# Optimization experiments

Measured on AMD Instinct MI355X. Metric: run time of the kernel, lower is better.

Reference implementation:

```python
import jax, jax.numpy as jnp
import numpy as np

B, P = 16, 1024
D_TIME, NUM_MODS = 8, 22
DIM_S = NUM_MODS + D_TIME + 1  # 31
PHI_W, N_HEADS, DP = 32, 4, 32
PSI_W, PSI_L, RHO_W = 64, 64, 64
SQRT_DP = float(np.sqrt(DP))


def setup_inputs() -> dict:
    key = jax.random.key(0)
    ks = jax.random.split(key, 16)
    rn = lambda k, shape: jax.random.normal(k, shape, jnp.float32) * 0.05
    return dict(
        times=jax.random.uniform(ks[0], (B, P), jnp.float32) * 48.0,
        values=jax.random.normal(ks[1], (B, P), jnp.float32),
        measurements=jax.random.randint(ks[2], (B, P), 0, NUM_MODS + 1),
        non_pad_mask=jnp.ones((B, P, 1), jnp.float32),
        W_psi1=rn(ks[3], (DIM_S, PSI_W)), b_psi1=jnp.zeros((PSI_W,), jnp.float32),
        W_psi2=rn(ks[4], (PSI_W, PSI_L)), b_psi2=jnp.zeros((PSI_L,), jnp.float32),
        W_key=rn(ks[5], (DIM_S + PSI_L, N_HEADS * DP)), b_key=jnp.zeros((N_HEADS * DP,), jnp.float32),
        query=rn(ks[6], (N_HEADS, DP)),
        W_phi1=rn(ks[7], (DIM_S, PHI_W)), b_phi1=jnp.zeros((PHI_W,), jnp.float32),
        W_phi2=rn(ks[8], (PHI_W, PHI_W)), b_phi2=jnp.zeros((PHI_W,), jnp.float32),
        W_rho1=rn(ks[9], (N_HEADS * PHI_W, RHO_W)), b_rho1=jnp.zeros((RHO_W,), jnp.float32),
        W_rho2=rn(ks[10], (RHO_W, RHO_W)), b_rho2=jnp.zeros((RHO_W,), jnp.float32),
    )


def _temporal_enc(times):
    i = np.arange(D_TIME)
    pos_vec = jnp.asarray(10000.0 ** (2.0 * (i // 2) / D_TIME), jnp.float32)
    ang = times[:, :, None] / pos_vec  # [B,P,d_time]
    return jnp.where(jnp.asarray(i % 2 == 0), jnp.sin(ang), jnp.cos(ang))


def reference(times, values, measurements, non_pad_mask,
              W_psi1, b_psi1, W_psi2, b_psi2, W_key, b_key, query,
              W_phi1, b_phi1, W_phi2, b_phi2, W_rho1, b_rho1, W_rho2, b_rho2):
    m = non_pad_mask  # [B,P,1]
    te = _temporal_enc(times)
    oh = jax.nn.one_hot(measurements, NUM_MODS + 1, dtype=jnp.float32)[:, :, 1:]
    x = jnp.concatenate([te, values[:, :, None], oh], axis=-1)  # [B,P,dim_s]

    # CumulativeSetAttentionLayer: psi MLP -> cumulative mean -> keys . query
    psi = jax.nn.relu(jax.nn.relu(x @ W_psi1 + b_psi1) @ W_psi2 + b_psi2)  # [B,P,psi_l]
    cum = jnp.cumsum(psi * m, axis=1) / jnp.cumsum(m, axis=1)
    keys = (jnp.concatenate([x, cum], axis=-1) @ W_key + b_key).reshape(B, P, N_HEADS, DP)
    pre = jnp.einsum('bpmd,md->bpm', keys, query) / SQRT_DP  # [B,P,m]

    # phi MLP
    phi = jax.nn.relu(jax.nn.relu(x @ W_phi1 + b_phi1) @ W_phi2 + b_phi2) * m  # [B,P,phi_w]

    # cumulative softmax weighting (online path)
    cmax = jax.lax.cummax(pre, axis=1)  # [B,P,m], running max for stability
    D = jnp.exp(pre[:, None, :, :] - cmax[:, :, None, :])  # [B,P,Q,m]
    causal = jnp.arange(P)[:, None] >= jnp.arange(P)[None, :]  # keep Q <= P
    D = D * causal[None, :, :, None]
    E = D.sum(axis=2)  # [B,P,m]
    agg = jnp.einsum('bpqm,bqd->bpmd', D, phi) / E[:, :, :, None]
    agg = (agg * m[:, :, :, None]).reshape(B, P, N_HEADS * PHI_W)

    # rho MLP (return_sequences)
    out = jax.nn.relu(jax.nn.relu(agg @ W_rho1 + b_rho1) @ W_rho2 + b_rho2) * m
    return out
```

## Files before the change

kernel.cpp:

```cpp
#include <hip/hip_runtime.h>
#include <hip/hip_bf16.h>

#define B_ 16
#define P_ 1024
#define T_ (B_*P_)
#define CH_ 32
#define CL_ (P_/CH_)

constexpr int OFF_A     = 16;
constexpr int OFF_WPSI1 = 400;
constexpr int OFF_BPSI1 = OFF_WPSI1 + 1984;
constexpr int OFF_WPSI2 = OFF_BPSI1 + 64;
constexpr int OFF_BPSI2 = OFF_WPSI2 + 4096;
constexpr int OFF_WPHI1 = OFF_BPSI2 + 64;
constexpr int OFF_BPHI1 = OFF_WPHI1 + 992;
constexpr int OFF_WPHI2 = OFF_BPHI1 + 32;
constexpr int OFF_BPHI2 = OFF_WPHI2 + 1024;
constexpr int OFF_WRHO1 = OFF_BPHI2 + 32;
constexpr int OFF_BRHO1 = OFF_WRHO1 + 8192;
constexpr int OFF_WRHO2 = OFF_BRHO1 + 64;
constexpr int OFF_BRHO2 = OFF_WRHO2 + 4096;
constexpr int OFF_PHI   = OFF_BRHO2 + 64;
constexpr int OFF_Z     = OFF_PHI   + T_*32;
constexpr int OFF_PREX  = OFF_Z     + T_*4;
constexpr int OFF_EXPW  = OFF_PREX  + T_*4;
constexpr int OFF_CE    = OFF_EXPW  + T_*4;
constexpr int OFF_CS    = OFF_CE    + 2048;

static __device__ __forceinline__ bool detect_f32(const void* mask_raw) {
  return ((*(const unsigned*)mask_raw) & 0xFFFFu) == 0u;
}
static __device__ __forceinline__ float ld_any(const void* src, int i, bool isf32) {
  if (isf32) return ((const float*)src)[i];
  return __bfloat162float(((const __hip_bfloat16*)src)[i]);
}

__global__ __launch_bounds__(256) void s01_prep(
    float* __restrict__ ws, const void* mask,
    const void* Wpsi1, const void* bpsi1, const void* Wpsi2, const void* bpsi2,
    const void* Wkey,  const void* bkey,  const void* query,
    const void* Wphi1, const void* bphi1, const void* Wphi2, const void* bphi2) {
  const bool isf32 = detect_f32(mask);
  if (blockIdx.x < 2) {
    const int gid = blockIdx.x * 256 + threadIdx.x;
    if (gid >= 384) return;
    const float inv_s = 0.17677669529663687f;
    const int h = gid & 3;
    const int j = gid >> 2;
    float s = 0.f;
    if (j < 95) {
      for (int d = 0; d < 32; ++d)
        s += ld_any(Wkey, j * 128 + h * 32 + d, isf32) * ld_any(query, h * 32 + d, isf32);
    } else {
      for (int d = 0; d < 32; ++d)
        s += ld_any(bkey, h * 32 + d, isf32) * ld_any(query, h * 32 + d, isf32);
    }
    ws[OFF_A + gid] = s * inv_s;
    return;
  }
  const int g  = (blockIdx.x - 2) * 256 + threadIdx.x;
  const int gs = (gridDim.x - 2) * 256;
  auto st = [&](int off, const void* src, int n) {
    for (int i = g; i < n; i += gs) ws[off + i] = ld_any(src, i, isf32);
  };
  st(OFF_WPSI1, Wpsi1, 1984); st(OFF_BPSI1, bpsi1, 64);
  st(OFF_WPSI2, Wpsi2, 4096); st(OFF_BPSI2, bpsi2, 64);
  st(OFF_WPHI1, Wphi1, 992);  st(OFF_BPHI1, bphi1, 32);
  st(OFF_WPHI2, Wphi2, 1024); st(OFF_BPHI2, bphi2, 32);
}

__global__ __launch_bounds__(256) void k1_token(float* __restrict__ ws,
                                                const int* __restrict__ measp,
                                                const void* __restrict__ times,
                                                const void* __restrict__ values,
                                                const void* __restrict__ mask) {
  __shared__ float sh1[4][64];
  __shared__ float sg1[4][32];
  const bool isf32 = detect_f32(mask);
  const int tid = threadIdx.x;
  const int wv  = __builtin_amdgcn_readfirstlane(tid >> 6);
  const int j   = tid & 63;
  const int t   = blockIdx.x * 4 + wv;

  const float tval = ld_any(times, t, isf32);
  const float vval = ld_any(values, t, isf32);
  const float mval = ld_any(mask, t, isf32);
  const int   meas = measp[t];
  const float sel  = (meas > 0) ? 1.f : 0.f;
  const int   mrow = (meas > 0) ? (8 + meas) : 0;

  float x[9];
  const float posv[4] = {1.f, 10.f, 100.f, 1000.f};
  #pragma unroll
  for (int k = 0; k < 4; ++k) {
    float s, c;
    __sincosf(tval / posv[k], &s, &c);
    x[2*k] = s; x[2*k+1] = c;
  }
  x[8] = vval;

  float h1 = ws[OFF_BPSI1 + j];
  #pragma unroll
  for (int i = 0; i < 9; ++i) h1 = fmaf(x[i], ws[OFF_WPSI1 + i * 64 + j], h1);
  h1 = fmaf(sel, ws[OFF_WPSI1 + mrow * 64 + j], h1);
  sh1[wv][j] = fmaxf(h1, 0.f);

  if (j < 32) {
    float g1 = ws[OFF_BPHI1 + j];
    #pragma unroll
    for (int i = 0; i < 9; ++i) g1 = fmaf(x[i], ws[OFF_WPHI1 + i * 32 + j], g1);
    g1 = fmaf(sel, ws[OFF_WPHI1 + mrow * 32 + j], g1);
    sg1[wv][j] = fmaxf(g1, 0.f);
  }
  __syncthreads();

  float h2 = ws[OFF_BPSI2 + j];
  #pragma unroll 8
  for (int i = 0; i < 64; ++i) h2 = fmaf(sh1[wv][i], ws[OFF_WPSI2 + i * 64 + j], h2);
  const float q = fmaxf(h2, 0.f) * mval;

  const float* a2 = ws + OFF_A + (31 + j) * 4;
  float z0 = q * a2[0], z1 = q * a2[1], z2 = q * a2[2], z3 = q * a2[3];
  #pragma unroll
  for (int off = 32; off; off >>= 1) {
    z0 += __shfl_xor(z0, off, 64);
    z1 += __shfl_xor(z1, off, 64);
    z2 += __shfl_xor(z2, off, 64);
    z3 += __shfl_xor(z3, off, 64);
  }
  if (j == 0) {
    float* zo = ws + OFF_Z + (size_t)t * 4;
    zo[0] = z0; zo[1] = z1; zo[2] = z2; zo[3] = z3;
  }

  if (j < 32) {
    float g2 = ws[OFF_BPHI2 + j];
    #pragma unroll 8
    for (int i = 0; i < 32; ++i) g2 = fmaf(sg1[wv][i], ws[OFF_WPHI2 + i * 32 + j], g2);
    ws[OFF_PHI + (size_t)t * 32 + j] = fmaxf(g2, 0.f) * mval;
  } else if (j < 36) {
    const int h = j - 32;
    float pr = ws[OFF_A + 380 + h];
    #pragma unroll
    for (int i = 0; i < 9; ++i) pr = fmaf(x[i], ws[OFF_A + i * 4 + h], pr);
    pr = fmaf(sel, ws[OFF_A + mrow * 4 + h], pr);
    ws[OFF_PREX + (size_t)t * 4 + h] = pr;
  }
}

__global__ __launch_bounds__(256) void k2_scanz(float* __restrict__ ws,
                                                const void* __restrict__ mask) {
  const int b    = blockIdx.x;
  const int tid  = threadIdx.x;
  const int lane = tid & 63;
  const int wv   = tid >> 6;
  const bool isf32 = detect_f32(mask);
  __shared__ float swt[4][5];
  __shared__ float smx[4][4];

  const float* zB = ws + OFF_Z + (size_t)b * P_ * 4;
  const int p0 = tid * 4;

  float lc[4], l0[4], l1[4], l2[4], l3[4];
  float c = 0.f, z0 = 0.f, z1 = 0.f, z2 = 0.f, z3 = 0.f;
  const float4* z4 = (const float4*)(zB + (size_t)p0 * 4);
  #pragma unroll
  for (int i = 0; i < 4; ++i) {
    const float4 zv = z4[i];
    c  += ld_any(mask, b * P_ + p0 + i, isf32);
    z0 += zv.x; z1 += zv.y; z2 += zv.z; z3 += zv.w;
    lc[i] = c; l0[i] = z0; l1[i] = z1; l2[i] = z2; l3[i] = z3;
  }

  float rc = c, r0 = z0, r1 = z1, r2 = z2, r3 = z3;
  #pragma unroll
  for (int off = 1; off < 64; off <<= 1) {
    const float uc = __shfl_up(rc, off, 64);
    const float u0 = __shfl_up(r0, off, 64);
    const float u1 = __shfl_up(r1, off, 64);
    const float u2 = __shfl_up(r2, off, 64);
    const float u3 = __shfl_up(r3, off, 64);
    if (lane >= off) { rc += uc; r0 += u0; r1 += u1; r2 += u2; r3 += u3; }
  }
  if (lane == 63) {
    swt[wv][0] = rc; swt[wv][1] = r0; swt[wv][2] = r1; swt[wv][3] = r2; swt[wv][4] = r3;
  }
  __syncthreads();
  #pragma unroll
  for (int w2 = 0; w2 < 3; ++w2) {
    if (wv > w2) {
      rc += swt[w2][0]; r0 += swt[w2][1]; r1 += swt[w2][2];
      r2 += swt[w2][3]; r3 += swt[w2][4];
    }
  }
  const float ec = rc - c, e0 = r0 - z0, e1 = r1 - z1, e2 = r2 - z2, e3 = r3 - z3;

  const float* px = ws + OFF_PREX + (size_t)b * P_ * 4;
  const float4* px4 = (const float4*)(px + (size_t)p0 * 4);
  float pre[4][4];
  float mx0 = -1e30f, mx1 = -1e30f, mx2 = -1e30f, mx3 = -1e30f;
  #pragma unroll
  for (int i = 0; i < 4; ++i) {
    const float inv = 1.f / (ec + lc[i]);
    const float4 pv = px4[i];
    pre[i][0] = pv.x + (e0 + l0[i]) * inv;
    pre[i][1] = pv.y + (e1 + l1[i]) * inv;
    pre[i][2] = pv.z + (e2 + l2[i]) * inv;
    pre[i][3] = pv.w + (e3 + l3[i]) * inv;
    mx0 = fmaxf(mx0, pre[i][0]); mx1 = fmaxf(mx1, pre[i][1]);
    mx2 = fmaxf(mx2, pre[i][2]); mx3 = fmaxf(mx3, pre[i][3]);
  }

  #pragma unroll
  for (int off = 32; off; off >>= 1) {
    mx0 = fmaxf(mx0, __shfl_xor(mx0, off, 64));
    mx1 = fmaxf(mx1, __shfl_xor(mx1, off, 64));
    mx2 = fmaxf(mx2, __shfl_xor(mx2, off, 64));
    mx3 = fmaxf(mx3, __shfl_xor(mx3, off, 64));
  }
  if (lane == 0) { smx[wv][0] = mx0; smx[wv][1] = mx1; smx[wv][2] = mx2; smx[wv][3] = mx3; }
  __syncthreads();
  const float M0 = fmaxf(fmaxf(smx[0][0], smx[1][0]), fmaxf(smx[2][0], smx[3][0]));
  const float M1 = fmaxf(fmaxf(smx[0][1], smx[1][1]), fmaxf(smx[2][1], smx[3][1]));
  const float M2 = fmaxf(fmaxf(smx[0][2], smx[1][2]), fmaxf(smx[2][2], smx[3][2]));
  const float M3 = fmaxf(fmaxf(smx[0][3], smx[1][3]), fmaxf(smx[2][3], smx[3][3]));

  float* eB = ws + OFF_EXPW + (size_t)b * P_ * 4;
  float4* e4 = (float4*)(eB + (size_t)p0 * 4);
  #pragma unroll
  for (int i = 0; i < 4; ++i) {
    float4 ev;
    ev.x = __expf(pre[i][0] - M0);
    ev.y = __expf(pre[i][1] - M1);
    ev.z = __expf(pre[i][2] - M2);
    ev.w = __expf(pre[i][3] - M3);
    e4[i] = ev;
  }
}

__global__ __launch_bounds__(128) void k4a_sums(float* __restrict__ ws) {
  const int ch = blockIdx.x, b = blockIdx.y;
  const int h = threadIdx.x >> 5, d = threadIdx.x & 31;
  const float* eB   = ws + OFF_EXPW + (size_t)b * P_ * 4;
  const float* phiB = ws + OFF_PHI  + (size_t)b * P_ * 32;

  float E = 0.f, S = 0.f;
  const int pbeg = ch * CL_;
  #pragma unroll 4
  for (int p = pbeg; p < pbeg + CL_; ++p) {
    const float e  = eB[p * 4 + h];
    const float ph = phiB[p * 32 + d];
    E += e;
    S = fmaf(e, ph, S);
  }
  const int base = (b * CH_ + ch) * 4 + h;
  if (d == 0) ws[OFF_CE + base] = E;
  ws[OFF_CS + base * 32 + d] = S;
}

__global__ __launch_bounds__(256) void k45_fused(float* __restrict__ ws,
    const void* __restrict__ mask,
    const void* __restrict__ Wrho1, const void* __restrict__ brho1,
    const void* __restrict__ Wrho2, const void* __restrict__ brho2,
    void* __restrict__ out) {
  __shared__ float sW1[8192];
  __shared__ float sAgg[32][128];
  __shared__ float sH1[32][64];
  const int ch = blockIdx.x, b = blockIdx.y;
  const int tid = threadIdx.x;
  const bool isf32 = detect_f32(mask);
  const int pbeg = ch * CL_;

  if (tid < 128) {
    const int h = tid >> 5, d = tid & 31;
    const float* eB   = ws + OFF_EXPW + (size_t)b * P_ * 4;
    const float* phiB = ws + OFF_PHI  + (size_t)b * P_ * 32;
    float E = 0.f, S = 0.f;
    for (int c2 = 0; c2 < ch; ++c2) {
      const int base2 = (b * CH_ + c2) * 4 + h;
      E += ws[OFF_CE + base2];
      S += ws[OFF_CS + base2 * 32 + d];
    }
    #pragma unroll 4
    for (int p = pbeg; p < pbeg + CL_; ++p) {
      const float e  = eB[p * 4 + h];
      const float ph = phiB[p * 32 + d];
      E += e;
      S = fmaf(e, ph, S);
      sAgg[p - pbeg][h * 32 + d] = (S / E) * ld_any(mask, b * P_ + p, isf32);
    }
  } else {
    for (int i = tid - 128; i < 8192; i += 128) sW1[i] = ld_any(Wrho1, i, isf32);
  }
  __syncthreads();

  const int j = tid & 63, qw = tid >> 6;
  const float b1 = ld_any(brho1, j, isf32);
  float acc[8];
  #pragma unroll
  for (int k = 0; k < 8; ++k) acc[k] = b1;
  for (int i4 = 0; i4 < 32; ++i4) {
    const float w0 = sW1[(i4 * 4 + 0) * 64 + j];
    const float w1 = sW1[(i4 * 4 + 1) * 64 + j];
    const float w2 = sW1[(i4 * 4 + 2) * 64 + j];
    const float w3 = sW1[(i4 * 4 + 3) * 64 + j];
    #pragma unroll
    for (int k = 0; k < 8; ++k) {
      const float4 a = *(const float4*)&sAgg[qw * 8 + k][i4 * 4];
      acc[k] = fmaf(a.w, w3, fmaf(a.z, w2, fmaf(a.y, w1, fmaf(a.x, w0, acc[k]))));
    }
  }
  #pragma unroll
  for (int k = 0; k < 8; ++k) sH1[qw * 8 + k][j] = fmaxf(acc[k], 0.f);
  __syncthreads();

  const float b2 = ld_any(brho2, j, isf32);
  float o[8];
  #pragma unroll
  for (int k = 0; k < 8; ++k) o[k] = b2;
  if (isf32) {
    const float* W2 = (const float*)Wrho2;
    #pragma unroll 4
    for (int i = 0; i < 64; ++i) {
      const float w = W2[i * 64 + j];
      #pragma unroll
      for (int k = 0; k < 8; ++k) o[k] = fmaf(sH1[qw * 8 + k][i], w, o[k]);
    }
  } else {
    const __hip_bfloat16* W2 = (const __hip_bfloat16*)Wrho2;
    #pragma unroll 4
    for (int i = 0; i < 64; ++i) {
      const float w = __bfloat162float(W2[i * 64 + j]);
      #pragma unroll
      for (int k = 0; k < 8; ++k) o[k] = fmaf(sH1[qw * 8 + k][i], w, o[k]);
    }
  }

  const int t0 = b * P_ + pbeg + qw * 8;
  #pragma unroll
  for (int k = 0; k < 8; ++k) {
    const float mv = ld_any(mask, t0 + k, isf32);
    const float v  = fmaxf(o[k], 0.f) * mv;
    if (isf32) {
      ((float*)out)[(size_t)(t0 + k) * 64 + j] = v;
    } else {
      ((__hip_bfloat16*)out)[(size_t)(t0 + k) * 64 + j] = __float2bfloat16(v);
    }
  }
}

extern "C" void kernel_launch(void* const* d_in, const int* in_sizes, int n_in,
                              void* d_out, int out_size, void* d_ws, size_t ws_size,
                              hipStream_t stream) {
  const int* meas = (const int*)d_in[2];
  const void* times = d_in[0];
  const void* values = d_in[1];
  const void* mask = d_in[3];
  float* ws = (float*)d_ws;

  s01_prep<<<10, 256, 0, stream>>>(ws, mask,
                                   d_in[4], d_in[5], d_in[6], d_in[7],
                                   d_in[8], d_in[9], d_in[10],
                                   d_in[11], d_in[12], d_in[13], d_in[14]);
  k1_token<<<T_/4, 256, 0, stream>>>(ws, meas, times, values, mask);
  k2_scanz<<<B_, 256, 0, stream>>>(ws, mask);
  k4a_sums<<<dim3(CH_, B_), 128, 0, stream>>>(ws);
  k45_fused<<<dim3(CH_, B_), 256, 0, stream>>>(ws, mask,
                                               d_in[15], d_in[16], d_in[17], d_in[18],
                                               d_out);
}
```

Before: 153.4 us.

## Parallelise scan per chunk with atomic chunk sums and per-chunk softmax max

k1 now accumulates per-chunk sums of mask and z with atomics, so the scan no longer needs one block per batch. The scan kernel becomes a 32x16 grid that folds the chunk prefixes, scans its own 32 tokens, and uses a max local to the chunk. It also fuses the chunk E/S sums, removing the separate k4a kernel. k45 rescales each chunk's partial sums by exp(chunk max minus running max), in the style of online softmax. The Wrho1 staging into shared memory also switches to vectorised loads. This trades more atomic contention in k1 and extra exp work for wider parallelism and one fewer launch.

```diff
diff --git a/kernel.cpp b/kernel.cpp
--- a/kernel.cpp
+++ b/kernel.cpp
@@ -26,6 +26,8 @@
 constexpr int OFF_EXPW  = OFF_PREX  + T_*4;
 constexpr int OFF_CE    = OFF_EXPW  + T_*4;
 constexpr int OFF_CS    = OFF_CE    + 2048;
+constexpr int OFF_CZ    = OFF_CS    + 65536;
+constexpr int OFF_CM    = OFF_CZ    + 2560;
 
 static __device__ __forceinline__ bool detect_f32(const void* mask_raw) {
   return ((*(const unsigned*)mask_raw) & 0xFFFFu) == 0u;
@@ -33,6 +35,9 @@
 static __device__ __forceinline__ float ld_any(const void* src, int i, bool isf32) {
   if (isf32) return ((const float*)src)[i];
   return __bfloat162float(((const __hip_bfloat16*)src)[i]);
+}
+static __device__ __forceinline__ float bfbits(unsigned u) {
+  union { unsigned q; float f; } x; x.q = u << 16; return x.f;
 }
 
 __global__ __launch_bounds__(256) void s01_prep(
@@ -67,6 +72,7 @@
   st(OFF_WPSI2, Wpsi2, 4096); st(OFF_BPSI2, bpsi2, 64);
   st(OFF_WPHI1, Wphi1, 992);  st(OFF_BPHI1, bphi1, 32);
   st(OFF_WPHI2, Wphi2, 1024); st(OFF_BPHI2, bphi2, 32);
+  for (int i = g; i < 2560; i += gs) ws[OFF_CZ + i] = 0.f;
 }
 
 __global__ __launch_bounds__(256) void k1_token(float* __restrict__ ws,
@@ -131,6 +137,12 @@
   if (j == 0) {
     float* zo = ws + OFF_Z + (size_t)t * 4;
     zo[0] = z0; zo[1] = z1; zo[2] = z2; zo[3] = z3;
+    const int slot = (t >> 10) * CH_ + ((t & (P_ - 1)) >> 5);
+    atomicAdd(ws + OFF_CZ + 0 * 512 + slot, mval);
+    atomicAdd(ws + OFF_CZ + 1 * 512 + slot, z0);
+    atomicAdd(ws + OFF_CZ + 2 * 512 + slot, z1);
+    atomicAdd(ws + OFF_CZ + 3 * 512 + slot, z2);
+    atomicAdd(ws + OFF_CZ + 4 * 512 + slot, z3);
   }
 
   if (j < 32) {
@@ -148,110 +160,80 @@
   }
 }
 
-__global__ __launch_bounds__(256) void k2_scanz(float* __restrict__ ws,
+__global__ __launch_bounds__(128) void k2b_scan(float* __restrict__ ws,
                                                 const void* __restrict__ mask) {
-  const int b    = blockIdx.x;
-  const int tid  = threadIdx.x;
-  const int lane = tid & 63;
-  const int wv   = tid >> 6;
+  const int ch = blockIdx.x, b = blockIdx.y;
+  const int tid = threadIdx.x;
   const bool isf32 = detect_f32(mask);
-  __shared__ float swt[4][5];
-  __shared__ float smx[4][4];
-
-  const float* zB = ws + OFF_Z + (size_t)b * P_ * 4;
-  const int p0 = tid * 4;
-
-  float lc[4], l0[4], l1[4], l2[4], l3[4];
-  float c = 0.f, z0 = 0.f, z1 = 0.f, z2 = 0.f, z3 = 0.f;
-  const float4* z4 = (const float4*)(zB + (size_t)p0 * 4);
-  #pragma unroll
-  for (int i = 0; i < 4; ++i) {
-    const float4 zv = z4[i];
-    c  += ld_any(mask, b * P_ + p0 + i, isf32);
-    z0 += zv.x; z1 += zv.y; z2 += zv.z; z3 += zv.w;
-    lc[i] = c; l0[i] = z0; l1[i] = z1; l2[i] = z2; l3[i] = z3;
-  }
-
-  float rc = c, r0 = z0, r1 = z1, r2 = z2, r3 = z3;
-  #pragma unroll
-  for (int off = 1; off < 64; off <<= 1) {
-    const float uc = __shfl_up(rc, off, 64);
-    const float u0 = __shfl_up(r0, off, 64);
-    const float u1 = __shfl_up(r1, off, 64);
-    const float u2 = __shfl_up(r2, off, 64);
-    const float u3 = __shfl_up(r3, off, 64);
-    if (lane >= off) { rc += uc; r0 += u0; r1 += u1; r2 += u2; r3 += u3; }
-  }
-  if (lane == 63) {
-    swt[wv][0] = rc; swt[wv][1] = r0; swt[wv][2] = r1; swt[wv][3] = r2; swt[wv][4] = r3;
+  __shared__ float sE[32][4];
+  const int pbeg = ch * CL_;
+
+  if (tid < 32) {
+    const int p = tid;
+    float pc = 0.f, p0 = 0.f, p1 = 0.f, p2 = 0.f, p3 = 0.f;
+    if (p < ch) {
+      const int s = b * CH_ + p;
+      pc = ws[OFF_CZ + 0 * 512 + s];
+      p0 = ws[OFF_CZ + 1 * 512 + s];
+      p1 = ws[OFF_CZ + 2 * 512 + s];
+      p2 = ws[OFF_CZ + 3 * 512 + s];
+      p3 = ws[OFF_CZ + 4 * 512 + s];
+    }
+    #pragma unroll
+    for (int mm = 16; mm; mm >>= 1) {
+      pc += __shfl_xor(pc, mm, 32);
+      p0 += __shfl_xor(p0, mm, 32);
+      p1 += __shfl_xor(p1, mm, 32);
+      p2 += __shfl_xor(p2, mm, 32);
+      p3 += __shfl_xor(p3, mm, 32);
+    }
+    const int tglob = b * P_ + pbeg + p;
+    float c = ld_any(mask, tglob, isf32);
+    const float4 zv = *(const float4*)(ws + OFF_Z + (size_t)tglob * 4);
+    float z0 = zv.x, z1 = zv.y, z2 = zv.z, z3 = zv.w;
+    #pragma unroll
+    for (int off = 1; off < 32; off <<= 1) {
+      const float uc = __shfl_up(c,  off, 32);
+      const float u0 = __shfl_up(z0, off, 32);
+      const float u1 = __shfl_up(z1, off, 32);
+      const float u2 = __shfl_up(z2, off, 32);
+      const float u3 = __shfl_up(z3, off, 32);
+      if (p >= off) { c += uc; z0 += u0; z1 += u1; z2 += u2; z3 += u3; }
+    }
+    const float inv = 1.f / (pc + c);
+    const float4 pxv = *(const float4*)(ws + OFF_PREX + (size_t)tglob * 4);
+    const float pr0 = pxv.x + (p0 + z0) * inv;
+    const float pr1 = pxv.y + (p1 + z1) * inv;
+    const float pr2 = pxv.z + (p2 + z2) * inv;
+    const float pr3 = pxv.w + (p3 + z3) * inv;
+    float m0 = pr0, m1 = pr1, m2 = pr2, m3 = pr3;
+    #pragma unroll
+    for (int mm = 16; mm; mm >>= 1) {
+      m0 = fmaxf(m0, __shfl_xor(m0, mm, 32));
+      m1 = fmaxf(m1, __shfl_xor(m1, mm, 32));
+      m2 = fmaxf(m2, __shfl_xor(m2, mm, 32));
+      m3 = fmaxf(m3, __shfl_xor(m3, mm, 32));
+    }
+    float4 ev;
+    ev.x = __expf(pr0 - m0); ev.y = __expf(pr1 - m1);
+    ev.z = __expf(pr2 - m2); ev.w = __expf(pr3 - m3);
+    *(float4*)(ws + OFF_EXPW + (size_t)tglob * 4) = ev;
+    sE[p][0] = ev.x; sE[p][1] = ev.y; sE[p][2] = ev.z; sE[p][3] = ev.w;
+    if (p == 0) {
+      float* cm = ws + OFF_CM + (size_t)(b * CH_ + ch) * 4;
+      cm[0] = m0; cm[1] = m1; cm[2] = m2; cm[3] = m3;
+    }
   }
   __syncthreads();
-  #pragma unroll
-  for (int w2 = 0; w2 < 3; ++w2) {
-    if (wv > w2) {
-      rc += swt[w2][0]; r0 += swt[w2][1]; r1 += swt[w2][2];
-      r2 += swt[w2][3]; r3 += swt[w2][4];
-    }
-  }
-  const float ec = rc - c, e0 = r0 - z0, e1 = r1 - z1, e2 = r2 - z2, e3 = r3 - z3;
-
-  const float* px = ws + OFF_PREX + (size_t)b * P_ * 4;
-  const float4* px4 = (const float4*)(px + (size_t)p0 * 4);
-  float pre[4][4];
-  float mx0 = -1e30f, mx1 = -1e30f, mx2 = -1e30f, mx3 = -1e30f;
-  #pragma unroll
-  for (int i = 0; i < 4; ++i) {
-    const float inv = 1.f / (ec + lc[i]);
-    const float4 pv = px4[i];
-    pre[i][0] = pv.x + (e0 + l0[i]) * inv;
-    pre[i][1] = pv.y + (e1 + l1[i]) * inv;
-    pre[i][2] = pv.z + (e2 + l2[i]) * inv;
-    pre[i][3] = pv.w + (e3 + l3[i]) * inv;
-    mx0 = fmaxf(mx0, pre[i][0]); mx1 = fmaxf(mx1, pre[i][1]);
-    mx2 = fmaxf(mx2, pre[i][2]); mx3 = fmaxf(mx3, pre[i][3]);
-  }
-
-  #pragma unroll
-  for (int off = 32; off; off >>= 1) {
-    mx0 = fmaxf(mx0, __shfl_xor(mx0, off, 64));
-    mx1 = fmaxf(mx1, __shfl_xor(mx1, off, 64));
-    mx2 = fmaxf(mx2, __shfl_xor(mx2, off, 64));
-    mx3 = fmaxf(mx3, __shfl_xor(mx3, off, 64));
-  }
-  if (lane == 0) { smx[wv][0] = mx0; smx[wv][1] = mx1; smx[wv][2] = mx2; smx[wv][3] = mx3; }
-  __syncthreads();
-  const float M0 = fmaxf(fmaxf(smx[0][0], smx[1][0]), fmaxf(smx[2][0], smx[3][0]));
-  const float M1 = fmaxf(fmaxf(smx[0][1], smx[1][1]), fmaxf(smx[2][1], smx[3][1]));
-  const float M2 = fmaxf(fmaxf(smx[0][2], smx[1][2]), fmaxf(smx[2][2], smx[3][2]));
-  const float M3 = fmaxf(fmaxf(smx[0][3], smx[1][3]), fmaxf(smx[2][3], smx[3][3]));
-
-  float* eB = ws + OFF_EXPW + (size_t)b * P_ * 4;
-  float4* e4 = (float4*)(eB + (size_t)p0 * 4);
-  #pragma unroll
-  for (int i = 0; i < 4; ++i) {
-    float4 ev;
-    ev.x = __expf(pre[i][0] - M0);
-    ev.y = __expf(pre[i][1] - M1);
-    ev.z = __expf(pre[i][2] - M2);
-    ev.w = __expf(pre[i][3] - M3);
-    e4[i] = ev;
-  }
-}
-
-__global__ __launch_bounds__(128) void k4a_sums(float* __restrict__ ws) {
-  const int ch = blockIdx.x, b = blockIdx.y;
-  const int h = threadIdx.x >> 5, d = threadIdx.x & 31;
-  const float* eB   = ws + OFF_EXPW + (size_t)b * P_ * 4;
-  const float* phiB = ws + OFF_PHI  + (size_t)b * P_ * 32;
-
+
+  const int h = tid >> 5, d = tid & 31;
+  const float* phiB = ws + OFF_PHI + (size_t)b * P_ * 32 + (size_t)pbeg * 32;
   float E = 0.f, S = 0.f;
-  const int pbeg = ch * CL_;
   #pragma unroll 4
-  for (int p = pbeg; p < pbeg + CL_; ++p) {
-    const float e  = eB[p * 4 + h];
-    const float ph = phiB[p * 32 + d];
+  for (int p = 0; p < 32; ++p) {
+    const float e = sE[p][h];
     E += e;
-    S = fmaf(e, ph, S);
+    S = fmaf(e, phiB[p * 32 + d], S);
   }
   const int base = (b * CH_ + ch) * 4 + h;
   if (d == 0) ws[OFF_CE + base] = E;
@@ -275,22 +257,47 @@
     const int h = tid >> 5, d = tid & 31;
     const float* eB   = ws + OFF_EXPW + (size_t)b * P_ * 4;
     const float* phiB = ws + OFF_PHI  + (size_t)b * P_ * 32;
+    const float* cmB  = ws + OFF_CM   + (size_t)b * CH_ * 4;
+
+    const float Mown = cmB[ch * 4 + h];
+    float Mst = Mown;
+    for (int c2 = 0; c2 < ch; ++c2) Mst = fmaxf(Mst, cmB[c2 * 4 + h]);
+
     float E = 0.f, S = 0.f;
     for (int c2 = 0; c2 < ch; ++c2) {
+      const float f = __expf(cmB[c2 * 4 + h] - Mst);
       const int base2 = (b * CH_ + c2) * 4 + h;
-      E += ws[OFF_CE + base2];
-      S += ws[OFF_CS + base2 * 32 + d];
-    }
+      E = fmaf(ws[OFF_CE + base2], f, E);
+      S = fmaf(ws[OFF_CS + base2 * 32 + d], f, S);
+    }
+    const float fo = __expf(Mown - Mst);
     #pragma unroll 4
     for (int p = pbeg; p < pbeg + CL_; ++p) {
-      const float e  = eB[p * 4 + h];
+      const float e  = eB[p * 4 + h] * fo;
       const float ph = phiB[p * 32 + d];
       E += e;
       S = fmaf(e, ph, S);
       sAgg[p - pbeg][h * 32 + d] = (S / E) * ld_any(mask, b * P_ + p, isf32);
     }
   } else {
-    for (int i = tid - 128; i < 8192; i += 128) sW1[i] = ld_any(Wrho1, i, isf32);
+    if (isf32) {
+      const float4* w1 = (const float4*)Wrho1;
+      for (int i = tid - 128; i < 2048; i += 128) {
+        const float4 v = w1[i];
+        float* dst = sW1 + i * 4;
+        dst[0] = v.x; dst[1] = v.y; dst[2] = v.z; dst[3] = v.w;
+      }
+    } else {
+      const uint4* w1 = (const uint4*)Wrho1;
+      for (int i = tid - 128; i < 1024; i += 128) {
+        const uint4 v = w1[i];
+        float* dst = sW1 + i * 8;
+        dst[0] = bfbits(v.x & 0xFFFFu); dst[1] = bfbits(v.x >> 16);
+        dst[2] = bfbits(v.y & 0xFFFFu); dst[3] = bfbits(v.y >> 16);
+        dst[4] = bfbits(v.z & 0xFFFFu); dst[5] = bfbits(v.z >> 16);
+        dst[6] = bfbits(v.w & 0xFFFFu); dst[7] = bfbits(v.w >> 16);
+      }
+    }
   }
   __syncthreads();
 
@@ -363,8 +370,7 @@
                                    d_in[8], d_in[9], d_in[10],
                                    d_in[11], d_in[12], d_in[13], d_in[14]);
   k1_token<<<T_/4, 256, 0, stream>>>(ws, meas, times, values, mask);
-  k2_scanz<<<B_, 256, 0, stream>>>(ws, mask);
-  k4a_sums<<<dim3(CH_, B_), 128, 0, stream>>>(ws);
+  k2b_scan<<<dim3(CH_, B_), 128, 0, stream>>>(ws, mask);
   k45_fused<<<dim3(CH_, B_), 256, 0, stream>>>(ws, mask,
                                                d_in[15], d_in[16], d_in[17], d_in[18],
                                                d_out);
```

New measurement: 181.9 us. 1.19x slower.

## Stage token MLP weights in LDS and process two tokens per wave

Applied to the files above, without the earlier changes.

The per-token MLP kernel now copies the psi/phi weights into shared memory once per block and has each wave compute two tokens, so every weight load feeds two FMAs. The block grows to 512 threads covering 16 tokens, which cuts redundant global/L2 weight reads but uses about 37 KB of LDS per block and may lower occupancy. Separately, the rho1 weight staging in the fused kernel switches to vectorized float4/uint4 loads with manual bf16 unpacking.

```diff
diff --git a/kernel.cpp b/kernel.cpp
--- a/kernel.cpp
+++ b/kernel.cpp
@@ -34,6 +34,9 @@
   if (isf32) return ((const float*)src)[i];
   return __bfloat162float(((const __hip_bfloat16*)src)[i]);
 }
+static __device__ __forceinline__ float bfbits(unsigned u) {
+  union { unsigned q; float f; } x; x.q = u << 16; return x.f;
+}
 
 __global__ __launch_bounds__(256) void s01_prep(
     float* __restrict__ ws, const void* mask,
@@ -69,80 +72,127 @@
   st(OFF_WPHI2, Wphi2, 1024); st(OFF_BPHI2, bphi2, 32);
 }
 
-__global__ __launch_bounds__(256) void k1_token(float* __restrict__ ws,
+__global__ __launch_bounds__(512) void k1_token(float* __restrict__ ws,
                                                 const int* __restrict__ measp,
                                                 const void* __restrict__ times,
                                                 const void* __restrict__ values,
                                                 const void* __restrict__ mask) {
-  __shared__ float sh1[4][64];
-  __shared__ float sg1[4][32];
+  __shared__ float sWS[8288];
+  __shared__ float sh1[16][64];
+  __shared__ float sg1[16][32];
+  constexpr int LW1 = 0, LB1 = 1984, LW2 = 2048, LB2 = 6144;
+  constexpr int LP1 = 6208, LQ1 = 7200, LP2 = 7232, LQ2 = 8256;
   const bool isf32 = detect_f32(mask);
   const int tid = threadIdx.x;
   const int wv  = __builtin_amdgcn_readfirstlane(tid >> 6);
   const int j   = tid & 63;
-  const int t   = blockIdx.x * 4 + wv;
-
-  const float tval = ld_any(times, t, isf32);
-  const float vval = ld_any(values, t, isf32);
-  const float mval = ld_any(mask, t, isf32);
-  const int   meas = measp[t];
-  const float sel  = (meas > 0) ? 1.f : 0.f;
-  const int   mrow = (meas > 0) ? (8 + meas) : 0;
-
-  float x[9];
+  const int ta  = blockIdx.x * 16 + wv * 2;
+  const int tb  = ta + 1;
+
+  const float tva = ld_any(times, ta, isf32),  tvb = ld_any(times, tb, isf32);
+  const float vva = ld_any(values, ta, isf32), vvb = ld_any(values, tb, isf32);
+  const float mva = ld_any(mask, ta, isf32),   mvb = ld_any(mask, tb, isf32);
+  const int   mea = measp[ta],                 meb = measp[tb];
+
+  {
+    const float4* src = (const float4*)(ws + OFF_WPSI1);
+    float4* dst = (float4*)sWS;
+    #pragma unroll
+    for (int i = tid; i < 2072; i += 512) dst[i] = src[i];
+  }
+
+  const float sea = (mea > 0) ? 1.f : 0.f;
+  const float seb = (meb > 0) ? 1.f : 0.f;
+  const int   mra = (mea > 0) ? (8 + mea) : 0;
+  const int   mrb = (meb > 0) ? (8 + meb) : 0;
+
+  float xa[9], xb[9];
   const float posv[4] = {1.f, 10.f, 100.f, 1000.f};
   #pragma unroll
   for (int k = 0; k < 4; ++k) {
     float s, c;
-    __sincosf(tval / posv[k], &s, &c);
-    x[2*k] = s; x[2*k+1] = c;
-  }
-  x[8] = vval;
-
-  float h1 = ws[OFF_BPSI1 + j];
-  #pragma unroll
-  for (int i = 0; i < 9; ++i) h1 = fmaf(x[i], ws[OFF_WPSI1 + i * 64 + j], h1);
-  h1 = fmaf(sel, ws[OFF_WPSI1 + mrow * 64 + j], h1);
-  sh1[wv][j] = fmaxf(h1, 0.f);
+    __sincosf(tva / posv[k], &s, &c); xa[2*k] = s; xa[2*k+1] = c;
+    __sincosf(tvb / posv[k], &s, &c); xb[2*k] = s; xb[2*k+1] = c;
+  }
+  xa[8] = vva; xb[8] = vvb;
+  __syncthreads();
+
+  float h1a = sWS[LB1 + j], h1b = h1a;
+  #pragma unroll
+  for (int i = 0; i < 9; ++i) {
+    const float w = sWS[LW1 + i * 64 + j];
+    h1a = fmaf(xa[i], w, h1a);
+    h1b = fmaf(xb[i], w, h1b);
+  }
+  h1a = fmaf(sea, sWS[LW1 + mra * 64 + j], h1a);
+  h1b = fmaf(seb, sWS[LW1 + mrb * 64 + j], h1b);
+  sh1[wv * 2 + 0][j] = fmaxf(h1a, 0.f);
+  sh1[wv * 2 + 1][j] = fmaxf(h1b, 0.f);
 
   if (j < 32) {
-    float g1 = ws[OFF_BPHI1 + j];
+    float g1a = sWS[LQ1 + j], g1b = g1a;
     #pragma unroll
-    for (int i = 0; i < 9; ++i) g1 = fmaf(x[i], ws[OFF_WPHI1 + i * 32 + j], g1);
-    g1 = fmaf(sel, ws[OFF_WPHI1 + mrow * 32 + j], g1);
-    sg1[wv][j] = fmaxf(g1, 0.f);
-  }
-  __syncthreads();
-
-  float h2 = ws[OFF_BPSI2 + j];
+    for (int i = 0; i < 9; ++i) {
+      const float w = sWS[LP1 + i * 32 + j];
+      g1a = fmaf(xa[i], w, g1a);
+      g1b = fmaf(xb[i], w, g1b);
+    }
+    g1a = fmaf(sea, sWS[LP1 + mra * 32 + j], g1a);
+    g1b = fmaf(seb, sWS[LP1 + mrb * 32 + j], g1b);
+    sg1[wv * 2 + 0][j] = fmaxf(g1a, 0.f);
+    sg1[wv * 2 + 1][j] = fmaxf(g1b, 0.f);
+  }
+  __syncthreads();
+
+  float h2a = sWS[LB2 + j], h2b = h2a;
   #pragma unroll 8
-  for (int i = 0; i < 64; ++i) h2 = fmaf(sh1[wv][i], ws[OFF_WPSI2 + i * 64 + j], h2);
-  const float q = fmaxf(h2, 0.f) * mval;
-
-  const float* a2 = ws + OFF_A + (31 + j) * 4;
-  float z0 = q * a2[0], z1 = q * a2[1], z2 = q * a2[2], z3 = q * a2[3];
+  for (int i = 0; i < 64; ++i) {
+    const float w = sWS[LW2 + i * 64 + j];
+    h2a = fmaf(sh1[wv * 2 + 0][i], w, h2a);
+    h2b = fmaf(sh1[wv * 2 + 1][i], w, h2b);
+  }
+  const float qa = fmaxf(h2a, 0.f) * mva;
+  const float qb = fmaxf(h2b, 0.f) * mvb;
+
+  const float4 a2 = *(const float4*)(ws + OFF_A + (31 + j) * 4);
+  float z0a = qa * a2.x, z1a = qa * a2.y, z2a = qa * a2.z, z3a = qa * a2.w;
+  float z0b = qb * a2.x, z1b = qb * a2.y, z2b = qb * a2.z, z3b = qb * a2.w;
   #pragma unroll
   for (int off = 32; off; off >>= 1) {
-    z0 += __shfl_xor(z0, off, 64);
-    z1 += __shfl_xor(z1, off, 64);
-    z2 += __shfl_xor(z2, off, 64);
-    z3 += __shfl_xor(z3, off, 64);
+    z0a += __shfl_xor(z0a, off, 64); z1a += __shfl_xor(z1a, off, 64);
+    z2a += __shfl_xor(z2a, off, 64); z3a += __shfl_xor(z3a, off, 64);
+    z0b += __shfl_xor(z0b, off, 64); z1b += __shfl_xor(z1b, off, 64);
+    z2b += __shfl_xor(z2b, off, 64); z3b += __shfl_xor(z3b, off, 64);
   }
   if (j == 0) {
-    float* zo = ws + OFF_Z + (size_t)t * 4;
-    zo[0] = z0; zo[1] = z1; zo[2] = z2; zo[3] = z3;
+    float4 va; va.x = z0a; va.y = z1a; va.z = z2a; va.w = z3a;
+    float4 vb; vb.x = z0b; vb.y = z1b; vb.z = z2b; vb.w = z3b;
+    *(float4*)(ws + OFF_Z + (size_t)ta * 4) = va;
+    *(float4*)(ws + OFF_Z + (size_t)tb * 4) = vb;
   }
 
   if (j < 32) {
-    float g2 = ws[OFF_BPHI2 + j];
+    float g2a = sWS[LQ2 + j], g2b = g2a;
     #pragma unroll 8
-    for (int i = 0; i < 32; ++i) g2 = fmaf(sg1[wv][i], ws[OFF_WPHI2 + i * 32 + j], g2);
-    ws[OFF_PHI + (size_t)t * 32 + j] = fmaxf(g2, 0.f) * mval;
-  } else if (j < 36) {
-    const int h = j - 32;
+    for (int i = 0; i < 32; ++i) {
+      const float w = sWS[LP2 + i * 32 + j];
+      g2a = fmaf(sg1[wv * 2 + 0][i], w, g2a);
+      g2b = fmaf(sg1[wv * 2 + 1][i], w, g2b);
+    }
+    ws[OFF_PHI + (size_t)ta * 32 + j] = fmaxf(g2a, 0.f) * mva;
+    ws[OFF_PHI + (size_t)tb * 32 + j] = fmaxf(g2b, 0.f) * mvb;
+  } else if (j < 40) {
+    const bool sec = j >= 36;
+    const int h = (j - 32) & 3;
+    const float sel  = sec ? seb : sea;
+    const int   mrow = sec ? mrb : mra;
+    const int   t    = sec ? tb : ta;
     float pr = ws[OFF_A + 380 + h];
     #pragma unroll
-    for (int i = 0; i < 9; ++i) pr = fmaf(x[i], ws[OFF_A + i * 4 + h], pr);
+    for (int i = 0; i < 9; ++i) {
+      const float xi = sec ? xb[i] : xa[i];
+      pr = fmaf(xi, ws[OFF_A + i * 4 + h], pr);
+    }
     pr = fmaf(sel, ws[OFF_A + mrow * 4 + h], pr);
     ws[OFF_PREX + (size_t)t * 4 + h] = pr;
   }
@@ -290,7 +340,24 @@
       sAgg[p - pbeg][h * 32 + d] = (S / E) * ld_any(mask, b * P_ + p, isf32);
     }
   } else {
-    for (int i = tid - 128; i < 8192; i += 128) sW1[i] = ld_any(Wrho1, i, isf32);
+    if (isf32) {
+      const float4* w1 = (const float4*)Wrho1;
+      for (int i = tid - 128; i < 2048; i += 128) {
+        const float4 v = w1[i];
+        float* dst = sW1 + i * 4;
+        dst[0] = v.x; dst[1] = v.y; dst[2] = v.z; dst[3] = v.w;
+      }
+    } else {
+      const uint4* w1 = (const uint4*)Wrho1;
+      for (int i = tid - 128; i < 1024; i += 128) {
+        const uint4 v = w1[i];
+        float* dst = sW1 + i * 8;
+        dst[0] = bfbits(v.x & 0xFFFFu); dst[1] = bfbits(v.x >> 16);
+        dst[2] = bfbits(v.y & 0xFFFFu); dst[3] = bfbits(v.y >> 16);
+        dst[4] = bfbits(v.z & 0xFFFFu); dst[5] = bfbits(v.z >> 16);
+        dst[6] = bfbits(v.w & 0xFFFFu); dst[7] = bfbits(v.w >> 16);
+      }
+    }
   }
   __syncthreads();
 
@@ -362,7 +429,7 @@
                                    d_in[4], d_in[5], d_in[6], d_in[7],
                                    d_in[8], d_in[9], d_in[10],
                                    d_in[11], d_in[12], d_in[13], d_in[14]);
-  k1_token<<<T_/4, 256, 0, stream>>>(ws, meas, times, values, mask);
+  k1_token<<<T_/16, 512, 0, stream>>>(ws, meas, times, values, mask);
   k2_scanz<<<B_, 256, 0, stream>>>(ws, mask);
   k4a_sums<<<dim3(CH_, B_), 128, 0, stream>>>(ws);
   k45_fused<<<dim3(CH_, B_), 256, 0, stream>>>(ws, mask,
```

After: 147.0 us. 1.04x faster.
